# Performance work log

Hardware: AMD Instinct MI355X
Metric: run time of the kernel (lower is better)

Reference implementation:

```python
import jax, jax.numpy as jnp
import numpy as np

B, T, C, H = 4, 4096, 1024, 64  # batch, seq, input_size, head_size


def setup_inputs() -> dict:
    key = jax.random.key(0)
    ks = jax.random.split(key, 7)
    s = 1.0 / np.sqrt(C)  # nn.Linear default init scale (uniform +-1/sqrt(fan_in))
    return {
        "x": jax.random.normal(ks[0], (B, T, C), dtype=jnp.float32),
        "Wk": jax.random.uniform(ks[1], (C, H), jnp.float32, -s, s),
        "bk": jax.random.uniform(ks[2], (H,), jnp.float32, -s, s),
        "Wq": jax.random.uniform(ks[3], (C, H), jnp.float32, -s, s),
        "bq": jax.random.uniform(ks[4], (H,), jnp.float32, -s, s),
        "Wv": jax.random.uniform(ks[5], (C, H), jnp.float32, -s, s),
        "bv": jax.random.uniform(ks[6], (H,), jnp.float32, -s, s),
    }


def reference(x, Wk, bk, Wq, bq, Wv, bv):
    b, t, c = x.shape
    k = x @ Wk + bk            # [B,T,H]
    q = x @ Wq + bq            # [B,T,H]
    v = x @ Wv + bv            # [B,T,H]
    # NOTE: original scales by C**-0.5 (input dim), not head_size**-0.5
    wei = jnp.einsum("bqh,bkh->bqk", q, k) * (c ** -0.5)  # [B,T,T]
    causal = jnp.tril(jnp.ones((t, t), dtype=bool))
    wei = jnp.where(causal, wei, -jnp.inf)
    wei = jax.nn.softmax(wei, axis=-1)
    # dropout p=0.0 (eval-mode baseline) -> identity
    return wei @ v             # [B,T,H]
```

## Files before the change

### kernel.cpp

```cpp
#include <hip/hip_runtime.h>

#define B_ 4
#define T_ 4096
#define C_ 1024
#define H_ 64
#define QSCALE 0.045084220027780106f

typedef float  f32x4  __attribute__((ext_vector_type(4)));
typedef float  f32x2  __attribute__((ext_vector_type(2)));
typedef __bf16 bf16x8 __attribute__((ext_vector_type(8)));
typedef __bf16 bf16x4 __attribute__((ext_vector_type(4)));

#define MFMA16(a, b, c) __builtin_amdgcn_mfma_f32_16x16x32_bf16((a), (b), (c), 0, 0, 0)

__device__ __forceinline__ void gl16(const void* g, void* l) {
    __builtin_amdgcn_global_load_lds(
        (const __attribute__((address_space(1))) void*)g,
        (__attribute__((address_space(3))) void*)l, 16, 0, 0);
}

#define CPB 187
#define NCHUNK 6

__global__ __launch_bounds__(256) void prep_wt(const float* __restrict__ Wk,
                                               const float* __restrict__ Wq,
                                               const float* __restrict__ Wv,
                                               __bf16* __restrict__ Wt) {
    __shared__ float tile[16][65];
    int tid = threadIdx.x;
    int mat = blockIdx.x >> 6;
    int k0  = (blockIdx.x & 63) * 16;
    const float* W = (mat == 0) ? Wk : ((mat == 1) ? Wq : Wv);
#pragma unroll
    for (int i = 0; i < 4; ++i) {
        int e = i * 256 + tid;
        int ki = e >> 6, n = e & 63;
        tile[ki][n] = W[(size_t)(k0 + ki) * 64 + n];
    }
    __syncthreads();
#pragma unroll
    for (int i = 0; i < 4; ++i) {
        int e = i * 256 + tid;
        int n = e >> 4, kj = e & 15;
        Wt[(size_t)mat * 65536 + (size_t)n * 1024 + k0 + kj] = (__bf16)tile[kj][n];
    }
}

#define STAGE(xd, wd, kk) do {                                              \
    const char* xs_ = xsrc + (size_t)(kk) * 4;                              \
    gl16(xs_,          (xd) + wq * 1024);                                   \
    gl16(xs_ + 65536,  (xd) + 4096 + wq * 1024);                            \
    const char* ws_ = wsrc + (size_t)(kk) * 2;                              \
    gl16(ws_,           (wd) + wq * 1024);                                  \
    gl16(ws_ + 65536,   (wd) + 4096  + wq * 1024);                          \
    gl16(ws_ + 131072,  (wd) + 8192  + wq * 1024);                          \
    gl16(ws_ + 196608,  (wd) + 12288 + wq * 1024);                          \
    gl16(ws_ + 262144,  (wd) + 16384 + wq * 1024);                          \
    gl16(ws_ + 327680,  (wd) + 20480 + wq * 1024);                          \
} while (0)

__global__ __launch_bounds__(256) void proj_qkv(const float* __restrict__ x,
                                                const __bf16* __restrict__ Wt,
                                                const float* __restrict__ bk,
                                                const float* __restrict__ bq,
                                                const float* __restrict__ bv,
                                                __bf16* __restrict__ Kg,
                                                __bf16* __restrict__ Qg,
                                                __bf16* __restrict__ Vt) {
    __shared__ char smem[65536];

    int tid  = threadIdx.x;
    int wq   = tid >> 6;
    int lane = tid & 63;
    int lo = lane & 15, g = lane >> 4;
    int swz = lo & 7;
    int w2 = wq >> 1, wc = wq & 1;
    int r0 = w2 * 16, n0 = wc * 96;
    int row0 = blockIdx.x * 32;

    const char* xsrc = (const char*)(x + (size_t)(row0 + (tid >> 4)) * C_
                                       + (size_t)(((tid & 15) ^ ((tid >> 4) & 7)) * 4));
    const char* wsrc = (const char*)Wt + (size_t)(tid >> 3) * 2048
                                       + (size_t)(((tid & 7) ^ ((tid >> 3) & 7)) * 16);

    char* xcur = smem;          char* xnxt = smem + 8192;
    char* wcur = smem + 16384;  char* wnxt = smem + 40960;

    f32x4 acc[6];
#pragma unroll
    for (int nt = 0; nt < 6; ++nt) acc[nt] = (f32x4){0.f, 0.f, 0.f, 0.f};

    STAGE(xcur, wcur, 0);
    __syncthreads();

#pragma unroll 1
    for (int step = 0; step < 16; ++step) {
        if (step < 15) STAGE(xnxt, wnxt, (step + 1) * 64);

        bf16x8 af[2];
        const char* ap = xcur + (r0 + lo) * 256;
#pragma unroll
        for (int kc = 0; kc < 2; ++kc) {
            int ch0 = kc * 8 + g * 2;
            f32x4 a0 = *(const f32x4*)(ap + ((ch0)     ^ swz) * 16);
            f32x4 a1 = *(const f32x4*)(ap + ((ch0 + 1) ^ swz) * 16);
            bf16x8 t;
            t[0] = (__bf16)a0[0]; t[1] = (__bf16)a0[1];
            t[2] = (__bf16)a0[2]; t[3] = (__bf16)a0[3];
            t[4] = (__bf16)a1[0]; t[5] = (__bf16)a1[1];
            t[6] = (__bf16)a1[2]; t[7] = (__bf16)a1[3];
            af[kc] = t;
        }
#pragma unroll
        for (int nt = 0; nt < 6; ++nt) {
            const char* bp_ = wcur + (n0 + nt * 16 + lo) * 128;
#pragma unroll
            for (int kc = 0; kc < 2; ++kc) {
                bf16x8 bf_ = *(const bf16x8*)(bp_ + ((kc * 4 + g) ^ swz) * 16);
                acc[nt] = MFMA16(af[kc], bf_, acc[nt]);
            }
        }
        __syncthreads();
        char* t1 = xcur; xcur = xnxt; xnxt = t1;
        char* t2 = wcur; wcur = wnxt; wnxt = t2;
    }

    int b_   = row0 >> 12;
    int tloc = row0 & (T_ - 1);
#pragma unroll
    for (int nt = 0; nt < 6; ++nt) {
        int col = n0 + nt * 16 + lo;
        int mat = col >> 6, h = col & 63;
        const float* bp = (mat == 0) ? bk : ((mat == 1) ? bq : bv);
        float bb = bp[h];
        if (mat == 2) {
            bf16x4 pv;
#pragma unroll
            for (int r = 0; r < 4; ++r) pv[r] = (__bf16)(acc[nt][r] + bb);
            *(bf16x4*)(Vt + (size_t)(b_ * 64 + h) * T_ + tloc + r0 + 4 * g) = pv;
        } else if (mat == 1) {
#pragma unroll
            for (int r = 0; r < 4; ++r)
                Qg[(size_t)(row0 + r0 + 4 * g + r) * H_ + h] = (__bf16)((acc[nt][r] + bb) * QSCALE);
        } else {
#pragma unroll
            for (int r = 0; r < 4; ++r)
                Kg[(size_t)(row0 + r0 + 4 * g + r) * H_ + h] = (__bf16)(acc[nt][r] + bb);
        }
    }
}

__device__ __forceinline__ void attn_iter_lds(const char* __restrict__ kb_,
                                              const char* __restrict__ vb_,
                                              int k0abs, int q0, bool domask,
                                              bf16x8 qb0, bf16x8 qb1,
                                              f32x4 (&acc)[4], float& m, float& l,
                                              char* pl, int lo, int g) {
    f32x4 st[4];
#pragma unroll
    for (int kt = 0; kt < 4; ++kt) {
        int row = kt * 16 + lo, sw = row & 7;
        bf16x8 ka0 = *(const bf16x8*)(kb_ + row * 128 + ((g ^ sw) << 4));
        bf16x8 ka1 = *(const bf16x8*)(kb_ + row * 128 + (((g + 4) ^ sw) << 4));
        f32x4 z = (f32x4){0.f, 0.f, 0.f, 0.f};
        __builtin_amdgcn_s_setprio(1);
        z = MFMA16(ka0, qb0, z);
        z = MFMA16(ka1, qb1, z);
        __builtin_amdgcn_s_setprio(0);
        st[kt] = z;
    }
    if (domask) {
#pragma unroll
        for (int kt = 0; kt < 4; ++kt)
#pragma unroll
            for (int r = 0; r < 4; ++r) {
                int kabs = k0abs + kt * 16 + 4 * g + r;
                if (kabs > q0 + lo) st[kt][r] = -1e30f;
            }
    }
    float mloc = -1e30f;
#pragma unroll
    for (int kt = 0; kt < 4; ++kt)
#pragma unroll
        for (int r = 0; r < 4; ++r) mloc = fmaxf(mloc, st[kt][r]);
    mloc = fmaxf(mloc, __shfl_xor(mloc, 16));
    mloc = fmaxf(mloc, __shfl_xor(mloc, 32));
    float mnew  = fmaxf(m, mloc);
    float alpha = exp2f(m - mnew);
    float ls = 0.f;
#pragma unroll
    for (int kt = 0; kt < 4; ++kt)
#pragma unroll
        for (int r = 0; r < 4; ++r) {
            float pe = exp2f(st[kt][r] - mnew);
            st[kt][r] = pe;
            ls += pe;
        }
    ls += __shfl_xor(ls, 16);
    ls += __shfl_xor(ls, 32);
    l = l * alpha + ls;
    m = mnew;
#pragma unroll
    for (int r = 0; r < 4; ++r) {
        float ar = __shfl(alpha, 4 * g + r);
#pragma unroll
        for (int ht = 0; ht < 4; ++ht) acc[ht][r] *= ar;
    }
#pragma unroll
    for (int kt = 0; kt < 4; ++kt) {
        bf16x4 pk;
#pragma unroll
        for (int r = 0; r < 4; ++r) pk[r] = (__bf16)st[kt][r];
        int waddr = (lo * 128 + kt * 32 + g * 8) ^ ((lo & 7) << 4);
        *(bf16x4*)(pl + waddr) = pk;
    }
#pragma unroll
    for (int c2 = 0; c2 < 2; ++c2) {
        int raddr = (lo * 128 + c2 * 64 + g * 16) ^ ((lo & 7) << 4);
        bf16x8 pa = *(const bf16x8*)(pl + raddr);
        __builtin_amdgcn_s_setprio(1);
#pragma unroll
        for (int ht = 0; ht < 4; ++ht) {
            int row = ht * 16 + lo, sw = row & 7;
            bf16x8 vb = *(const bf16x8*)(vb_ + row * 128 + (((c2 * 4 + g) ^ sw) << 4));
            acc[ht] = MFMA16(pa, vb, acc[ht]);
        }
        __builtin_amdgcn_s_setprio(0);
    }
}

__global__ __launch_bounds__(512) void attn_fwd(const __bf16* __restrict__ Qg,
                                                const __bf16* __restrict__ Kg,
                                                const __bf16* __restrict__ Vt,
                                                __bf16* __restrict__ partO,
                                                float* __restrict__ partML) {
    __shared__ alignas(16) char smem[49152];

    int tid  = threadIdx.x;
    int w    = tid >> 6;
    int lane = tid & 63;
    int lo = lane & 15, gq = lane >> 4;

    int bid = blockIdx.x;
    int b   = bid / CPB;
    int u   = bid - b * CPB;
    int g = 0, cum = 0;
#pragma unroll 1
    for (; g < 32; ++g) {
        int s = (2 * g + 7) / 6;
        if (u < cum + s) break;
        cum += s;
    }
    int c    = u - cum;
    int j0   = NCHUNK * c;
    int cnt  = min(NCHUNK, 2 * g + 2 - j0);
    int mydiag = 2 * g + (w >> 2);
    int q0   = g * 128 + w * 16;

    const char* kgb = (const char*)Kg + (size_t)b * 524288;
    const char* vgb = (const char*)Vt + (size_t)b * 524288;

    int sr = tid >> 3;
    int sc2 = (tid & 7) ^ (sr & 7);
    int koff = sr * 128 + sc2 * 16;
    int voff = sr * 8192 + sc2 * 16;
    char* pl = smem + 32768 + w * 2048;

    const __bf16* qp = Qg + (size_t)(b * T_ + q0 + lo) * H_ + gq * 8;
    bf16x8 qb0 = *(const bf16x8*)(qp);
    bf16x8 qb1 = *(const bf16x8*)(qp + 32);

    f32x4 acc[4];
#pragma unroll
    for (int ht = 0; ht < 4; ++ht) acc[ht] = (f32x4){0.f, 0.f, 0.f, 0.f};
    float m = -1e30f, l = 0.f;

    gl16(kgb + (size_t)j0 * 8192 + koff, smem + w * 1024);
    gl16(vgb + (size_t)j0 * 128 + voff, smem + 16384 + w * 1024);

#pragma unroll 1
    for (int t = 0; t < cnt; ++t) {
        __builtin_amdgcn_s_barrier();
        if (t + 1 < cnt) {
            int kb = j0 + t + 1;
            int nb = ((t + 1) & 1) * 8192;
            gl16(kgb + (size_t)kb * 8192 + koff, smem + nb + w * 1024);
            gl16(vgb + (size_t)kb * 128 + voff, smem + 16384 + nb + w * 1024);
            asm volatile("s_waitcnt vmcnt(2)" ::: "memory");
        } else {
            asm volatile("s_waitcnt vmcnt(0)" ::: "memory");
        }
        __builtin_amdgcn_s_barrier();
        __builtin_amdgcn_sched_barrier(0);
        int kb = j0 + t;
        if (kb <= mydiag)
            attn_iter_lds(smem + (t & 1) * 8192, smem + 16384 + (t & 1) * 8192,
                          kb * 64, q0, kb == mydiag,
                          qb0, qb1, acc, m, l, pl, lo, gq);
    }

    __bf16* po = partO + (size_t)bid * 8192;
#pragma unroll
    for (int ht = 0; ht < 4; ++ht)
#pragma unroll
        for (int r = 0; r < 4; ++r)
            po[(w * 16 + 4 * gq + r) * 64 + ht * 16 + lo] = (__bf16)acc[ht][r];
    if (gq == 0) {
        partML[bid * 256 + (w * 16 + lo) * 2 + 0] = m;
        partML[bid * 256 + (w * 16 + lo) * 2 + 1] = l;
    }
}

__global__ __launch_bounds__(256) void mergeN(const __bf16* __restrict__ partO,
                                              const float* __restrict__ partML,
                                              float* __restrict__ out) {
    int e = blockIdx.x * 256 + threadIdx.x;
    int row = e >> 6, h = e & 63;
    int b = row >> 12, rl = row & 4095;
    int g = rl >> 7, r128 = rl & 127;
    int cum = 0;
#pragma unroll 1
    for (int gg = 0; gg < g; ++gg) cum += (2 * gg + 7) / 6;
    int S = (2 * g + 7) / 6;
    int base = b * CPB + cum;

    float M = -1e30f, L = 0.f, O = 0.f;
#pragma unroll 1
    for (int c2 = 0; c2 < S; ++c2) {
        f32x2 mlv = *(const f32x2*)(partML + (base + c2) * 256 + r128 * 2);
        float oc = (float)partO[(size_t)(base + c2) * 8192 + r128 * 64 + h];
        float Mn = fmaxf(M, mlv[0]);
        float s0 = exp2f(M - Mn), s1 = exp2f(mlv[0] - Mn);
        L = L * s0 + mlv[1] * s1;
        O = O * s0 + oc * s1;
        M = Mn;
    }
    out[e] = O / L;
}

extern "C" void kernel_launch(void* const* d_in, const int* in_sizes, int n_in,
                              void* d_out, int out_size, void* d_ws, size_t ws_size,
                              hipStream_t stream) {
    const float* x  = (const float*)d_in[0];
    const float* Wk = (const float*)d_in[1];
    const float* bk = (const float*)d_in[2];
    const float* Wq = (const float*)d_in[3];
    const float* bq = (const float*)d_in[4];
    const float* Wv = (const float*)d_in[5];
    const float* bv = (const float*)d_in[6];

    char* ws = (char*)d_ws;
    __bf16* Wt = (__bf16*)(ws);
    __bf16* Kg = (__bf16*)(ws + 393216);
    __bf16* Qg = (__bf16*)(ws + 393216 + 2097152);
    __bf16* Vt = (__bf16*)(ws + 393216 + 2 * 2097152);
    __bf16* partO  = (__bf16*)(ws + 6684672);
    float*  partML = (float*)(ws + 6684672 + 12255232);
    float* out = (float*)d_out;

    prep_wt<<<192, 256, 0, stream>>>(Wk, Wq, Wv, Wt);
    proj_qkv<<<512, 256, 0, stream>>>(x, Wt, bk, bq, bv, Kg, Qg, Vt);
    attn_fwd<<<4 * CPB, 512, 0, stream>>>(Qg, Kg, Vt, partO, partML);
    mergeN<<<4096, 256, 0, stream>>>(partO, partML, out);
}
```

Baseline: 62.13 us.

## Switch attention to 32x32 MFMA with register-resident P and 4-wave blocks

```diff
diff --git a/kernel.cpp b/kernel.cpp
--- a/kernel.cpp
+++ b/kernel.cpp
@@ -6,17 +6,26 @@
 #define H_ 64
 #define QSCALE 0.045084220027780106f
 
-typedef float  f32x4  __attribute__((ext_vector_type(4)));
-typedef float  f32x2  __attribute__((ext_vector_type(2)));
-typedef __bf16 bf16x8 __attribute__((ext_vector_type(8)));
-typedef __bf16 bf16x4 __attribute__((ext_vector_type(4)));
+typedef float  f32x4   __attribute__((ext_vector_type(4)));
+typedef float  f32x2   __attribute__((ext_vector_type(2)));
+typedef float  f32x16  __attribute__((ext_vector_type(16)));
+typedef int    i32x4   __attribute__((ext_vector_type(4)));
+typedef __bf16 bf16x8  __attribute__((ext_vector_type(8)));
+typedef __bf16 bf16x4  __attribute__((ext_vector_type(4)));
 
 #define MFMA16(a, b, c) __builtin_amdgcn_mfma_f32_16x16x32_bf16((a), (b), (c), 0, 0, 0)
+#define MFMA32(a, b, c) __builtin_amdgcn_mfma_f32_32x32x16_bf16((a), (b), (c), 0, 0, 0)
 
 __device__ __forceinline__ void gl16(const void* g, void* l) {
     __builtin_amdgcn_global_load_lds(
         (const __attribute__((address_space(1))) void*)g,
         (__attribute__((address_space(3))) void*)l, 16, 0, 0);
+}
+
+__device__ __forceinline__ unsigned pk2(float a, float b) {
+    __bf16 ba = (__bf16)a, bb = (__bf16)b;
+    return (unsigned)__builtin_bit_cast(unsigned short, ba)
+         | ((unsigned)__builtin_bit_cast(unsigned short, bb) << 16);
 }
 
 #define CPB 187
@@ -150,96 +159,123 @@
     }
 }
 
-__device__ __forceinline__ void attn_iter_lds(const char* __restrict__ kb_,
-                                              const char* __restrict__ vb_,
-                                              int k0abs, int q0, bool domask,
-                                              bf16x8 qb0, bf16x8 qb1,
-                                              f32x4 (&acc)[4], float& m, float& l,
-                                              char* pl, int lo, int g) {
-    f32x4 st[4];
-#pragma unroll
-    for (int kt = 0; kt < 4; ++kt) {
-        int row = kt * 16 + lo, sw = row & 7;
-        bf16x8 ka0 = *(const bf16x8*)(kb_ + row * 128 + ((g ^ sw) << 4));
-        bf16x8 ka1 = *(const bf16x8*)(kb_ + row * 128 + (((g + 4) ^ sw) << 4));
-        f32x4 z = (f32x4){0.f, 0.f, 0.f, 0.f};
+__device__ __forceinline__ void attn_iter32(const char* __restrict__ kb_,
+                                            const char* __restrict__ vb_,
+                                            int k0abs, int q0abs, bool domask,
+                                            const bf16x8 (&qB)[4],
+                                            f32x16 (&accO)[2], float& m, float& l,
+                                            int lq, int h2) {
+    int sw = lq & 7;
+    f32x16 st[2];
+#pragma unroll
+    for (int kt = 0; kt < 2; ++kt) {
+        int row = kt * 32 + lq;
+        f32x16 z;
+#pragma unroll
+        for (int i = 0; i < 16; ++i) z[i] = 0.f;
         __builtin_amdgcn_s_setprio(1);
-        z = MFMA16(ka0, qb0, z);
-        z = MFMA16(ka1, qb1, z);
+#pragma unroll
+        for (int s = 0; s < 4; ++s) {
+            bf16x8 ka = *(const bf16x8*)(kb_ + row * 128 + (((2 * s + h2) ^ sw) << 4));
+            z = MFMA32(ka, qB[s], z);
+        }
         __builtin_amdgcn_s_setprio(0);
         st[kt] = z;
     }
     if (domask) {
 #pragma unroll
-        for (int kt = 0; kt < 4; ++kt)
-#pragma unroll
-            for (int r = 0; r < 4; ++r) {
-                int kabs = k0abs + kt * 16 + 4 * g + r;
-                if (kabs > q0 + lo) st[kt][r] = -1e30f;
+        for (int kt = 0; kt < 2; ++kt)
+#pragma unroll
+            for (int r = 0; r < 16; ++r) {
+                int kabs = k0abs + kt * 32 + (r & 3) + 8 * (r >> 2) + 4 * h2;
+                if (kabs > q0abs + lq) st[kt][r] = -1e30f;
             }
     }
     float mloc = -1e30f;
 #pragma unroll
-    for (int kt = 0; kt < 4; ++kt)
-#pragma unroll
-        for (int r = 0; r < 4; ++r) mloc = fmaxf(mloc, st[kt][r]);
-    mloc = fmaxf(mloc, __shfl_xor(mloc, 16));
+    for (int kt = 0; kt < 2; ++kt)
+#pragma unroll
+        for (int r = 0; r < 16; ++r) mloc = fmaxf(mloc, st[kt][r]);
     mloc = fmaxf(mloc, __shfl_xor(mloc, 32));
     float mnew  = fmaxf(m, mloc);
     float alpha = exp2f(m - mnew);
     float ls = 0.f;
 #pragma unroll
-    for (int kt = 0; kt < 4; ++kt)
-#pragma unroll
-        for (int r = 0; r < 4; ++r) {
+    for (int kt = 0; kt < 2; ++kt)
+#pragma unroll
+        for (int r = 0; r < 16; ++r) {
             float pe = exp2f(st[kt][r] - mnew);
             st[kt][r] = pe;
             ls += pe;
         }
-    ls += __shfl_xor(ls, 16);
     ls += __shfl_xor(ls, 32);
     l = l * alpha + ls;
     m = mnew;
 #pragma unroll
-    for (int r = 0; r < 4; ++r) {
-        float ar = __shfl(alpha, 4 * g + r);
-#pragma unroll
-        for (int ht = 0; ht < 4; ++ht) acc[ht][r] *= ar;
-    }
-#pragma unroll
-    for (int kt = 0; kt < 4; ++kt) {
-        bf16x4 pk;
-#pragma unroll
-        for (int r = 0; r < 4; ++r) pk[r] = (__bf16)st[kt][r];
-        int waddr = (lo * 128 + kt * 32 + g * 8) ^ ((lo & 7) << 4);
-        *(bf16x4*)(pl + waddr) = pk;
-    }
-#pragma unroll
-    for (int c2 = 0; c2 < 2; ++c2) {
-        int raddr = (lo * 128 + c2 * 64 + g * 16) ^ ((lo & 7) << 4);
-        bf16x8 pa = *(const bf16x8*)(pl + raddr);
+    for (int nt = 0; nt < 2; ++nt)
+#pragma unroll
+        for (int r = 0; r < 16; ++r) accO[nt][r] *= alpha;
+
+    int pk[16];
+#pragma unroll
+    for (int kt = 0; kt < 2; ++kt)
+#pragma unroll
+        for (int sg = 0; sg < 4; ++sg)
+#pragma unroll
+            for (int gm = 0; gm < 2; ++gm)
+                pk[kt * 8 + sg * 2 + gm] =
+                    (int)pk2(st[kt][4 * sg + 2 * gm], st[kt][4 * sg + 2 * gm + 1]);
+
+    bf16x8 pfrag[4];
+#pragma unroll
+    for (int s = 0; s < 4; ++s) {
+        int iA0 = ((2 * s) >> 2) * 8 + ((2 * s) & 3) * 2;
+        int iB0 = ((2 * s + 1) >> 2) * 8 + ((2 * s + 1) & 3) * 2;
+        int x0 = pk[iA0],     x1 = pk[iA0 + 1];
+        int z0 = pk[iB0],     z1 = pk[iB0 + 1];
+        int y0 = __shfl_xor(x0, 32), y1 = __shfl_xor(x1, 32);
+        int u0 = __shfl_xor(z0, 32), u1 = __shfl_xor(z1, 32);
+        int w0 = h2 ? u0 : x0;
+        int w1 = h2 ? u1 : x1;
+        int w2 = h2 ? z0 : y0;
+        int w3 = h2 ? z1 : y1;
+        i32x4 wv = (i32x4){w0, w1, w2, w3};
+        pfrag[s] = __builtin_bit_cast(bf16x8, wv);
+    }
+
+#pragma unroll
+    for (int nt = 0; nt < 2; ++nt) {
+        int row = nt * 32 + lq;
         __builtin_amdgcn_s_setprio(1);
 #pragma unroll
-        for (int ht = 0; ht < 4; ++ht) {
-            int row = ht * 16 + lo, sw = row & 7;
-            bf16x8 vb = *(const bf16x8*)(vb_ + row * 128 + (((c2 * 4 + g) ^ sw) << 4));
-            acc[ht] = MFMA16(pa, vb, acc[ht]);
+        for (int s = 0; s < 4; ++s) {
+            bf16x8 va = *(const bf16x8*)(vb_ + row * 128 + (((2 * s + h2) ^ sw) << 4));
+            accO[nt] = MFMA32(va, pfrag[s], accO[nt]);
         }
         __builtin_amdgcn_s_setprio(0);
     }
 }
 
-__global__ __launch_bounds__(512) void attn_fwd(const __bf16* __restrict__ Qg,
-                                                const __bf16* __restrict__ Kg,
-                                                const __bf16* __restrict__ Vt,
-                                                __bf16* __restrict__ partO,
-                                                float* __restrict__ partML) {
-    __shared__ alignas(16) char smem[49152];
+#define STAGE_KV(kb, buf) do {                                              \
+    const char* ks_ = kgb + (size_t)(kb) * 8192;                            \
+    const char* vs_ = vgb + (size_t)(kb) * 128;                             \
+    gl16(ks_ + koff0, smem + (buf) + wb);                                   \
+    gl16(ks_ + koff1, smem + (buf) + 4096 + wb);                            \
+    gl16(vs_ + voff0, smem + 16384 + (buf) + wb);                           \
+    gl16(vs_ + voff1, smem + 16384 + (buf) + 4096 + wb);                    \
+} while (0)
+
+__global__ __launch_bounds__(256, 4) void attn_fwd(const __bf16* __restrict__ Qg,
+                                                   const __bf16* __restrict__ Kg,
+                                                   const __bf16* __restrict__ Vt,
+                                                   __bf16* __restrict__ partO,
+                                                   float* __restrict__ partML) {
+    __shared__ alignas(16) char smem[32768];
 
     int tid  = threadIdx.x;
     int w    = tid >> 6;
     int lane = tid & 63;
-    int lo = lane & 15, gq = lane >> 4;
+    int lq = lane & 31, h2 = lane >> 5;
 
     int bid = blockIdx.x;
     int b   = bid / CPB;
@@ -254,39 +290,40 @@
     int c    = u - cum;
     int j0   = NCHUNK * c;
     int cnt  = min(NCHUNK, 2 * g + 2 - j0);
-    int mydiag = 2 * g + (w >> 2);
-    int q0   = g * 128 + w * 16;
+    int mydiag = 2 * g + (w >> 1);
+    int q0   = g * 128 + w * 32;
 
     const char* kgb = (const char*)Kg + (size_t)b * 524288;
     const char* vgb = (const char*)Vt + (size_t)b * 524288;
 
-    int sr = tid >> 3;
-    int sc2 = (tid & 7) ^ (sr & 7);
-    int koff = sr * 128 + sc2 * 16;
-    int voff = sr * 8192 + sc2 * 16;
-    char* pl = smem + 32768 + w * 2048;
-
-    const __bf16* qp = Qg + (size_t)(b * T_ + q0 + lo) * H_ + gq * 8;
-    bf16x8 qb0 = *(const bf16x8*)(qp);
-    bf16x8 qb1 = *(const bf16x8*)(qp + 32);
-
-    f32x4 acc[4];
-#pragma unroll
-    for (int ht = 0; ht < 4; ++ht) acc[ht] = (f32x4){0.f, 0.f, 0.f, 0.f};
+    int r8  = tid >> 3;
+    int sc2 = (tid & 7) ^ (r8 & 7);
+    size_t koff0 = (size_t)r8 * 128 + sc2 * 16;
+    size_t koff1 = (size_t)(r8 + 32) * 128 + sc2 * 16;
+    size_t voff0 = (size_t)r8 * 8192 + sc2 * 16;
+    size_t voff1 = (size_t)(r8 + 32) * 8192 + sc2 * 16;
+    int wb = w * 1024;
+
+    const __bf16* qp = Qg + (size_t)(b * T_ + q0 + lq) * H_ + 8 * h2;
+    bf16x8 qB[4];
+#pragma unroll
+    for (int s = 0; s < 4; ++s) qB[s] = *(const bf16x8*)(qp + 16 * s);
+
+    f32x16 accO[2];
+#pragma unroll
+    for (int nt = 0; nt < 2; ++nt)
+#pragma unroll
+        for (int i = 0; i < 16; ++i) accO[nt][i] = 0.f;
     float m = -1e30f, l = 0.f;
 
-    gl16(kgb + (size_t)j0 * 8192 + koff, smem + w * 1024);
-    gl16(vgb + (size_t)j0 * 128 + voff, smem + 16384 + w * 1024);
+    STAGE_KV(j0, 0);
 
 #pragma unroll 1
     for (int t = 0; t < cnt; ++t) {
         __builtin_amdgcn_s_barrier();
         if (t + 1 < cnt) {
-            int kb = j0 + t + 1;
-            int nb = ((t + 1) & 1) * 8192;
-            gl16(kgb + (size_t)kb * 8192 + koff, smem + nb + w * 1024);
-            gl16(vgb + (size_t)kb * 128 + voff, smem + 16384 + nb + w * 1024);
-            asm volatile("s_waitcnt vmcnt(2)" ::: "memory");
+            STAGE_KV(j0 + t + 1, ((t + 1) & 1) * 8192);
+            asm volatile("s_waitcnt vmcnt(4)" ::: "memory");
         } else {
             asm volatile("s_waitcnt vmcnt(0)" ::: "memory");
         }
@@ -294,20 +331,24 @@
         __builtin_amdgcn_sched_barrier(0);
         int kb = j0 + t;
         if (kb <= mydiag)
-            attn_iter_lds(smem + (t & 1) * 8192, smem + 16384 + (t & 1) * 8192,
-                          kb * 64, q0, kb == mydiag,
-                          qb0, qb1, acc, m, l, pl, lo, gq);
+            attn_iter32(smem + (t & 1) * 8192, smem + 16384 + (t & 1) * 8192,
+                        kb * 64, q0, kb == mydiag, qB, accO, m, l, lq, h2);
     }
 
     __bf16* po = partO + (size_t)bid * 8192;
-#pragma unroll
-    for (int ht = 0; ht < 4; ++ht)
-#pragma unroll
-        for (int r = 0; r < 4; ++r)
-            po[(w * 16 + 4 * gq + r) * 64 + ht * 16 + lo] = (__bf16)acc[ht][r];
-    if (gq == 0) {
-        partML[bid * 256 + (w * 16 + lo) * 2 + 0] = m;
-        partML[bid * 256 + (w * 16 + lo) * 2 + 1] = l;
+    int q = w * 32 + lq;
+#pragma unroll
+    for (int nt = 0; nt < 2; ++nt)
+#pragma unroll
+        for (int sg = 0; sg < 4; ++sg) {
+            bf16x4 pv;
+#pragma unroll
+            for (int cc = 0; cc < 4; ++cc) pv[cc] = (__bf16)accO[nt][4 * sg + cc];
+            *(bf16x4*)(po + q * 64 + nt * 32 + 8 * sg + 4 * h2) = pv;
+        }
+    if (h2 == 0) {
+        partML[bid * 256 + q * 2 + 0] = m;
+        partML[bid * 256 + q * 2 + 1] = l;
     }
 }
 
@@ -360,6 +401,6 @@
 
     prep_wt<<<192, 256, 0, stream>>>(Wk, Wq, Wv, Wt);
     proj_qkv<<<512, 256, 0, stream>>>(x, Wt, bk, bq, bv, Kg, Qg, Vt);
-    attn_fwd<<<4 * CPB, 512, 0, stream>>>(Qg, Kg, Vt, partO, partML);
+    attn_fwd<<<4 * CPB, 256, 0, stream>>>(Qg, Kg, Vt, partO, partML);
     mergeN<<<4096, 256, 0, stream>>>(partO, partML, out);
 }
```

Measured after the change: 65.03 us. +4.7%, slower.
